# Kernel optimization log

Hardware: AMD Instinct MI355X
Metric: run time of the kernel (lower is better)

## Reference

```python
import jax, jax.numpy as jnp
import numpy as np

N, IN_DIM, EDGE_DIM = 100000, 64, 16
E = 1600000
H, C = 4, 16  # heads, out_dim per head; H*C = 64
K = 3
NEG_SLOPE = 0.2
LN_EPS = 1e-5


def setup_inputs() -> dict:
    key = jax.random.key(0)
    ks = jax.random.split(key, 16)
    s = 1.0 / np.sqrt(IN_DIM)
    se = 1.0 / np.sqrt(EDGE_DIM)
    HC = H * C
    return {
        "x": jax.random.normal(ks[0], (N, IN_DIM), jnp.float32),
        "edge_index": jax.random.randint(ks[1], (2, E), 0, N, jnp.int32),
        "edge_attr": jax.random.normal(ks[2], (E, EDGE_DIM), jnp.float32),
        "dist_to_boundary": jax.random.randint(ks[3], (N,), 0, K + 1, jnp.int32),
        # GATv2Conv params
        "W_l": jax.random.normal(ks[4], (IN_DIM, HC), jnp.float32) * s,
        "b_l": jnp.zeros((HC,), jnp.float32),
        "W_r": jax.random.normal(ks[5], (IN_DIM, HC), jnp.float32) * s,
        "b_r": jnp.zeros((HC,), jnp.float32),
        "W_e": jax.random.normal(ks[6], (EDGE_DIM, HC), jnp.float32) * se,
        "att": jax.random.normal(ks[7], (H, C), jnp.float32) * (1.0 / np.sqrt(C)),
        "bias": jnp.zeros((HC,), jnp.float32),
        # LayerNorm params
        "gamma": jnp.ones((HC,), jnp.float32),
        "beta": jnp.zeros((HC,), jnp.float32),
        # residual: in_dim == H*C -> Identity in original; identity-initialized Linear
        "W_res": jnp.eye(IN_DIM, HC, dtype=jnp.float32),
        "b_res": jnp.zeros((HC,), jnp.float32),
        "bias_per_hop": jnp.zeros((K + 1,), jnp.float32),
    }


def reference(x, edge_index, edge_attr, dist_to_boundary,
              W_l, b_l, W_r, b_r, W_e, att, bias,
              gamma, beta, W_res, b_res, bias_per_hop):
    n = x.shape[0]
    src, dst = edge_index[0], edge_index[1]

    # hop bias on edge features (module indexes edge_index[1])
    hop = jnp.clip(dist_to_boundary[dst], 0, K)
    ea = edge_attr + bias_per_hop[hop][:, None] * 0.1  # [E, edge_dim]

    # GATv2Conv (eval mode: no dropout)
    xl = (x @ W_l + b_l).reshape(n, H, C)
    xr = (x @ W_r + b_r).reshape(n, H, C)
    ee = (ea @ W_e).reshape(-1, H, C)
    m = xl[src] + xr[dst] + ee                      # [E,H,C]
    m = jnp.where(m > 0, m, NEG_SLOPE * m)          # leaky_relu
    logits = jnp.einsum('ehc,hc->eh', m, att)       # [E,H]

    # segment softmax over destination nodes
    amax = jax.ops.segment_max(logits, dst, num_segments=n)
    ex = jnp.exp(logits - amax[dst])
    den = jax.ops.segment_sum(ex, dst, num_segments=n)
    alpha = ex / (den[dst] + 1e-16)                 # [E,H]

    # weighted scatter-add of source features
    out = jax.ops.segment_sum(alpha[:, :, None] * xl[src], dst, num_segments=n)
    out = out.reshape(n, H * C) + bias

    # LayerNorm
    mu = out.mean(-1, keepdims=True)
    var = ((out - mu) ** 2).mean(-1, keepdims=True)
    out = (out - mu) / jnp.sqrt(var + LN_EPS) * gamma + beta

    # residual (Identity in original since in_dim == H*C; W_res is identity)
    return out + (x @ W_res + b_res)
```

## Files before the change

### kernel.cpp

```cpp
#include <hip/hip_runtime.h>
#include <math.h>

#define NEG_SLOPE 0.2f
#define LN_EPS 1e-5f
#define BUCKET 48

typedef __attribute__((ext_vector_type(2))) float f32x2;

template <int CTRL>
__device__ __forceinline__ float dpp_add(float x) {
    int s = __builtin_amdgcn_update_dpp(0, __float_as_int(x), CTRL, 0xF, 0xF, true);
    return x + __int_as_float(s);
}
__device__ __forceinline__ float row16_sum(float x) {
    x = dpp_add<0xB1>(x);
    x = dpp_add<0x4E>(x);
    x = dpp_add<0x124>(x);
    x = dpp_add<0x128>(x);
    return x;
}

__global__ __launch_bounds__(256) void prep(
    const float* __restrict__ x,
    const float* __restrict__ W_l, const float* __restrict__ b_l,
    const float* __restrict__ W_r, const float* __restrict__ b_r,
    const float* __restrict__ W_res, const float* __restrict__ b_res,
    const float* __restrict__ W_e,
    const int* __restrict__ dist, const float* __restrict__ bph,
    float* __restrict__ xl, float* __restrict__ xr, float* __restrict__ xres_out,
    const int* __restrict__ ei, int* __restrict__ counts, int2* __restrict__ bucket,
    int n, int E_) {
    __shared__ float sWl[4096];
    __shared__ float sWr[4096];
    __shared__ float sWs[4096];
    __shared__ float sx[256];
    for (int i = threadIdx.x; i < 4096; i += 256) {
        sWl[i] = W_l[i]; sWr[i] = W_r[i]; sWs[i] = W_res[i];
    }
    int lane = threadIdx.x & 63;
    int w = threadIdx.x >> 6;
    float bl = b_l[lane], br = b_r[lane], bs = b_res[lane];
    float wsum = 0.0f;
#pragma unroll
    for (int k = 0; k < 16; ++k) wsum += W_e[k * 64 + lane];
    __syncthreads();
    for (int base = blockIdx.x * 4; base < n; base += gridDim.x * 4) {
        __syncthreads();
        int r = base + w;
        if (r < n) sx[threadIdx.x] = x[(size_t)r * 64 + lane];
        __syncthreads();
        if (r < n) {
            float al = bl, ar = br, as_ = bs;
            const float* xv = &sx[w * 64];
#pragma unroll
            for (int k = 0; k < 64; ++k) {
                float xk = xv[k];
                al = fmaf(xk, sWl[k * 64 + lane], al);
                ar = fmaf(xk, sWr[k * 64 + lane], ar);
                as_ = fmaf(xk, sWs[k * 64 + lane], as_);
            }
            int hop = dist[r];
            hop = hop < 0 ? 0 : (hop > 3 ? 3 : hop);
            float hb = 0.1f * bph[hop];
            xl[(size_t)r * 64 + lane] = al;
            xr[(size_t)r * 64 + lane] = fmaf(hb, wsum, ar);
            xres_out[(size_t)r * 64 + lane] = as_;
        }
    }
    const int* di = ei + E_;
    for (int e = blockIdx.x * 256 + threadIdx.x; e < E_; e += gridDim.x * 256) {
        int dst = di[e];
        int src = ei[e];
        int pos = atomicAdd(&counts[dst], 1);
        pos = pos < BUCKET - 1 ? pos : BUCKET - 1;
        bucket[(size_t)dst * BUCKET + pos] = make_int2(e, src);
    }
}

#define LOAD_G(G, EA)                                                       \
    {                                                                       \
        int ec = __builtin_amdgcn_readfirstlane((EA).x);                    \
        const f32x2* p = (const f32x2*)(eattr + (size_t)ec * 16);           \
        _Pragma("unroll") for (int k = 0; k < 8; ++k) G[k] = p[k];          \
    }

#define PHASE(G, X, E, DEN, ACC, I)                                         \
    {                                                                       \
        f32x2 mm; mm.x = X + base; mm.y = 0.0f;                             \
        _Pragma("unroll") for (int k = 0; k < 8; ++k)                       \
            mm = __builtin_elementwise_fma(G[k], w2[k], mm);                \
        float m = mm.x + mm.y;                                              \
        m = fmaxf(m, NEG_SLOPE * m);                                        \
        float l = row16_sum(m * attv);      \
        l = (I) < cnt ? l : -1e30f;                                         \
        float ex = __builtin_amdgcn_exp2f(l);                               \
        DEN += ex;                                                          \
        ACC = fmaf(ex, X, ACC);                                             \
        X = xl[((unsigned)(E).y << 6) | lane];                              \
        LOAD_G(G, E);                                                       \
        int nx = (I) + 6; nx = nx > last ? last : nx;                       \
        E = bk[nx];                                                         \
    }

__global__ __launch_bounds__(256) void fused_gather(
    const int* __restrict__ counts, const int2* __restrict__ bucket,
    const float* __restrict__ eattr,
    const float* __restrict__ W_e, const float* __restrict__ att,
    const float* __restrict__ xl, const float* __restrict__ xr,
    const float* __restrict__ bias,
    const float* __restrict__ gamma, const float* __restrict__ beta,
    float* out, int n) {
    int lane = threadIdx.x & 63;
    float attv = att[lane] * 1.44269504f;
    float bi = bias[lane], g = gamma[lane], be = beta[lane];
    f32x2 w2[8];
#pragma unroll
    for (int k = 0; k < 8; ++k) {
        w2[k].x = W_e[(2 * k) * 64 + lane];
        w2[k].y = W_e[(2 * k + 1) * 64 + lane];
    }

    int wid = (blockIdx.x * blockDim.x + threadIdx.x) >> 6;
    int nw = (gridDim.x * blockDim.x) >> 6;
    for (int r = wid; r < n; r += nw) {
        int cnt = counts[r];
        float den0 = 0.0f, den1 = 0.0f, den2 = 0.0f;
        float acc0 = 0.0f, acc1 = 0.0f, acc2 = 0.0f;
        if (cnt > 0) {
            cnt = cnt < BUCKET ? cnt : BUCKET;
            float base = xr[((unsigned)r << 6) | lane];
            const int2* bk = bucket + (size_t)r * BUCKET;
            int last = cnt - 1;
            int i1 = 1 > last ? last : 1;
            int i2 = 2 > last ? last : 2;
            int i3 = 3 > last ? last : 3;
            int i4 = 4 > last ? last : 4;
            int i5 = 5 > last ? last : 5;
            int2 A0 = bk[0];
            int2 A1 = bk[i1];
            int2 A2 = bk[i2];
            int2 E0 = bk[i3];
            int2 E1 = bk[i4];
            int2 E2 = bk[i5];
            float X0 = xl[((unsigned)A0.y << 6) | lane];
            float X1 = xl[((unsigned)A1.y << 6) | lane];
            float X2 = xl[((unsigned)A2.y << 6) | lane];
            f32x2 G0[8], G1[8], G2[8];
            LOAD_G(G0, A0);
            LOAD_G(G1, A1);
            LOAD_G(G2, A2);
            for (int i = 0; i < cnt; i += 3) {
                PHASE(G0, X0, E0, den0, acc0, i)
                PHASE(G1, X1, E1, den1, acc1, i + 1)
                PHASE(G2, X2, E2, den2, acc2, i + 2)
            }
        }
        float den = (den0 + den1) + den2;
        float acc = (acc0 + acc1) + acc2;
        float v = acc / (den + 1e-16f) + bi;
        float s = row16_sum(v);
        s += __shfl_xor(s, 16, 64);
        s += __shfl_xor(s, 32, 64);
        float mu = s * (1.0f / 64.0f);
        float dd = v - mu;
        float q = row16_sum(dd * dd);
        q += __shfl_xor(q, 16, 64);
        q += __shfl_xor(q, 32, 64);
        float var = q * (1.0f / 64.0f);
        float nv = dd * rsqrtf(var + LN_EPS) * g + be;
        unsigned idx = ((unsigned)r << 6) | lane;
        out[idx] = nv + out[idx];
    }
}

extern "C" void kernel_launch(void* const* d_in, const int* in_sizes, int n_in,
                              void* d_out, int out_size, void* d_ws, size_t ws_size,
                              hipStream_t stream) {
    const float* x     = (const float*)d_in[0];
    const int*   ei    = (const int*)d_in[1];
    const float* eattr = (const float*)d_in[2];
    const int*   dist  = (const int*)d_in[3];
    const float* W_l   = (const float*)d_in[4];
    const float* b_l   = (const float*)d_in[5];
    const float* W_r   = (const float*)d_in[6];
    const float* b_r   = (const float*)d_in[7];
    const float* W_e   = (const float*)d_in[8];
    const float* att   = (const float*)d_in[9];
    const float* bias  = (const float*)d_in[10];
    const float* gamma = (const float*)d_in[11];
    const float* beta  = (const float*)d_in[12];
    const float* W_res = (const float*)d_in[13];
    const float* b_res = (const float*)d_in[14];
    const float* bph   = (const float*)d_in[15];

    int n  = in_sizes[0] / 64;
    int E_ = in_sizes[1] / 2;
    float* out = (float*)d_out;

    char* ws = (char*)d_ws;
    float* xl     = (float*)ws; ws += (size_t)n * 64 * 4;
    float* xr     = (float*)ws; ws += (size_t)n * 64 * 4;
    int2*  bucket = (int2*)ws;  ws += (size_t)n * BUCKET * 8;
    int*   counts = (int*)ws;   ws += (size_t)n * 4;

    hipMemsetAsync(counts, 0, (size_t)n * 4, stream);
    prep<<<2048, 256, 0, stream>>>(x, W_l, b_l, W_r, b_r, W_res, b_res, W_e,
                                   dist, bph, xl, xr, out, ei, counts, bucket, n, E_);
    fused_gather<<<4096, 256, 0, stream>>>(counts, bucket, eattr,
                                           W_e, att, xl, xr,
                                           bias, gamma, beta, out, n);
}
```

Before: 279.8 us.

## Deepen xl gather prefetch and compute two rows per wave in prep

In the fused gather, the xl row for each edge is now fetched one iteration earlier than the edge-attribute load, using an extra prefetch stage (XA/XB plus E/F index pipeline, lookahead 9). The aim is to hide gather latency better in this latency-bound loop. In prep, each wave now handles two node rows, so every weight value read from LDS is reused twice and LDS traffic per FMA drops. The cost is higher register pressure in both kernels, which may lower occupancy.

```diff
diff --git a/kernel.cpp b/kernel.cpp
--- a/kernel.cpp
+++ b/kernel.cpp
@@ -33,7 +33,7 @@
     __shared__ float sWl[4096];
     __shared__ float sWr[4096];
     __shared__ float sWs[4096];
-    __shared__ float sx[256];
+    __shared__ float sx[512];
     for (int i = threadIdx.x; i < 4096; i += 256) {
         sWl[i] = W_l[i]; sWr[i] = W_r[i]; sWs[i] = W_res[i];
     }
@@ -44,27 +44,49 @@
 #pragma unroll
     for (int k = 0; k < 16; ++k) wsum += W_e[k * 64 + lane];
     __syncthreads();
-    for (int base = blockIdx.x * 4; base < n; base += gridDim.x * 4) {
+    for (int base = blockIdx.x * 8; base < n; base += gridDim.x * 8) {
         __syncthreads();
-        int r = base + w;
-        if (r < n) sx[threadIdx.x] = x[(size_t)r * 64 + lane];
+        {
+            int idx = threadIdx.x;
+            int row = base + (idx >> 6);
+            if (row < n) sx[idx] = x[(size_t)row * 64 + (idx & 63)];
+            idx += 256;
+            row = base + (idx >> 6);
+            if (row < n) sx[idx] = x[(size_t)row * 64 + (idx & 63)];
+        }
         __syncthreads();
-        if (r < n) {
-            float al = bl, ar = br, as_ = bs;
-            const float* xv = &sx[w * 64];
+        int ra = base + w * 2;
+        int rb = ra + 1;
+        if (ra < n) {
+            float al0 = bl, ar0 = br, as0 = bs;
+            float al1 = bl, ar1 = br, as1 = bs;
+            const float* xa = &sx[(w * 2) * 64];
 #pragma unroll
             for (int k = 0; k < 64; ++k) {
-                float xk = xv[k];
-                al = fmaf(xk, sWl[k * 64 + lane], al);
-                ar = fmaf(xk, sWr[k * 64 + lane], ar);
-                as_ = fmaf(xk, sWs[k * 64 + lane], as_);
-            }
-            int hop = dist[r];
-            hop = hop < 0 ? 0 : (hop > 3 ? 3 : hop);
-            float hb = 0.1f * bph[hop];
-            xl[(size_t)r * 64 + lane] = al;
-            xr[(size_t)r * 64 + lane] = fmaf(hb, wsum, ar);
-            xres_out[(size_t)r * 64 + lane] = as_;
+                float wl = sWl[k * 64 + lane];
+                float wr_ = sWr[k * 64 + lane];
+                float ws_ = sWs[k * 64 + lane];
+                float x0 = xa[k];
+                float x1 = xa[k + 64];
+                al0 = fmaf(x0, wl, al0); ar0 = fmaf(x0, wr_, ar0); as0 = fmaf(x0, ws_, as0);
+                al1 = fmaf(x1, wl, al1); ar1 = fmaf(x1, wr_, ar1); as1 = fmaf(x1, ws_, as1);
+            }
+            {
+                int hop = dist[ra];
+                hop = hop < 0 ? 0 : (hop > 3 ? 3 : hop);
+                float hb = 0.1f * bph[hop];
+                xl[(size_t)ra * 64 + lane] = al0;
+                xr[(size_t)ra * 64 + lane] = fmaf(hb, wsum, ar0);
+                xres_out[(size_t)ra * 64 + lane] = as0;
+            }
+            if (rb < n) {
+                int hop = dist[rb];
+                hop = hop < 0 ? 0 : (hop > 3 ? 3 : hop);
+                float hb = 0.1f * bph[hop];
+                xl[(size_t)rb * 64 + lane] = al1;
+                xr[(size_t)rb * 64 + lane] = fmaf(hb, wsum, ar1);
+                xres_out[(size_t)rb * 64 + lane] = as1;
+            }
         }
     }
     const int* di = ei + E_;
@@ -84,9 +106,9 @@
         _Pragma("unroll") for (int k = 0; k < 8; ++k) G[k] = p[k];          \
     }
 
-#define PHASE(G, X, E, DEN, ACC, I)                                         \
+#define PHASE(G, XA, XB, E, F, DEN, ACC, I)                                 \
     {                                                                       \
-        f32x2 mm; mm.x = X + base; mm.y = 0.0f;                             \
+        f32x2 mm; mm.x = XA + base; mm.y = 0.0f;                            \
         _Pragma("unroll") for (int k = 0; k < 8; ++k)                       \
             mm = __builtin_elementwise_fma(G[k], w2[k], mm);                \
         float m = mm.x + mm.y;                                              \
@@ -95,11 +117,13 @@
         l = (I) < cnt ? l : -1e30f;                                         \
         float ex = __builtin_amdgcn_exp2f(l);                               \
         DEN += ex;                                                          \
-        ACC = fmaf(ex, X, ACC);                                             \
-        X = xl[((unsigned)(E).y << 6) | lane];                              \
+        ACC = fmaf(ex, XA, ACC);                                            \
+        XA = XB;                                                            \
+        XB = xl[((unsigned)(F).y << 6) | lane];                             \
         LOAD_G(G, E);                                                       \
-        int nx = (I) + 6; nx = nx > last ? last : nx;                       \
-        E = bk[nx];                                                         \
+        E = F;                                                              \
+        int nx = (I) + 9; nx = nx > last ? last : nx;                       \
+        F = bk[nx];                                                         \
     }
 
 __global__ __launch_bounds__(256) void fused_gather(
@@ -131,28 +155,37 @@
             float base = xr[((unsigned)r << 6) | lane];
             const int2* bk = bucket + (size_t)r * BUCKET;
             int last = cnt - 1;
-            int i1 = 1 > last ? last : 1;
-            int i2 = 2 > last ? last : 2;
-            int i3 = 3 > last ? last : 3;
-            int i4 = 4 > last ? last : 4;
-            int i5 = 5 > last ? last : 5;
-            int2 A0 = bk[0];
-            int2 A1 = bk[i1];
-            int2 A2 = bk[i2];
-            int2 E0 = bk[i3];
-            int2 E1 = bk[i4];
-            int2 E2 = bk[i5];
-            float X0 = xl[((unsigned)A0.y << 6) | lane];
-            float X1 = xl[((unsigned)A1.y << 6) | lane];
-            float X2 = xl[((unsigned)A2.y << 6) | lane];
+            int j1 = 1 > last ? last : 1;
+            int j2 = 2 > last ? last : 2;
+            int j3 = 3 > last ? last : 3;
+            int j4 = 4 > last ? last : 4;
+            int j5 = 5 > last ? last : 5;
+            int j6 = 6 > last ? last : 6;
+            int j7 = 7 > last ? last : 7;
+            int j8 = 8 > last ? last : 8;
+            int2 B0 = bk[0];
+            int2 B1 = bk[j1];
+            int2 B2 = bk[j2];
+            int2 E0 = bk[j3];
+            int2 E1 = bk[j4];
+            int2 E2 = bk[j5];
+            int2 F0 = bk[j6];
+            int2 F1 = bk[j7];
+            int2 F2 = bk[j8];
+            float Xa0 = xl[((unsigned)B0.y << 6) | lane];
+            float Xa1 = xl[((unsigned)B1.y << 6) | lane];
+            float Xa2 = xl[((unsigned)B2.y << 6) | lane];
+            float Xb0 = xl[((unsigned)E0.y << 6) | lane];
+            float Xb1 = xl[((unsigned)E1.y << 6) | lane];
+            float Xb2 = xl[((unsigned)E2.y << 6) | lane];
             f32x2 G0[8], G1[8], G2[8];
-            LOAD_G(G0, A0);
-            LOAD_G(G1, A1);
-            LOAD_G(G2, A2);
+            LOAD_G(G0, B0);
+            LOAD_G(G1, B1);
+            LOAD_G(G2, B2);
             for (int i = 0; i < cnt; i += 3) {
-                PHASE(G0, X0, E0, den0, acc0, i)
-                PHASE(G1, X1, E1, den1, acc1, i + 1)
-                PHASE(G2, X2, E2, den2, acc2, i + 2)
+                PHASE(G0, Xa0, Xb0, E0, F0, den0, acc0, i)
+                PHASE(G1, Xa1, Xb1, E1, F1, den1, acc1, i + 1)
+                PHASE(G2, Xa2, Xb2, E2, F2, den2, acc2, i + 2)
             }
         }
         float den = (den0 + den1) + den2;
```

New measurement: 324.3 us. +15.9%, slower.

## Split fused gather into edge-order logit kernel and destination gather kernel

Applied to the files above, without the earlier changes.

The fused per-destination kernel is split in two. A new edge_logits kernel walks edges in their original order, so the edge_attr reads are contiguous, and writes exp(logit) per edge and head to a workspace buffer. A second kernel gathers those values together with xl rows per destination, then does the normalization and LayerNorm. The aim is to avoid random 64-byte edge_attr reads in the gather, at the cost of an extra kernel launch, a 25.6MB intermediate write and read, and random xr[dst] gathers in the edge pass.

```diff
diff --git a/kernel.cpp b/kernel.cpp
--- a/kernel.cpp
+++ b/kernel.cpp
@@ -77,49 +77,102 @@
     }
 }
 
-#define LOAD_G(G, EA)                                                       \
+#define CL(J) ((J) > last ? last : (J))
+
+#define LLOAD_G(G, EE)                                                      \
     {                                                                       \
-        int ec = __builtin_amdgcn_readfirstlane((EA).x);                    \
-        const f32x2* p = (const f32x2*)(eattr + (size_t)ec * 16);           \
+        const f32x2* p = (const f32x2*)(eattr + (size_t)(EE) * 16);         \
         _Pragma("unroll") for (int k = 0; k < 8; ++k) G[k] = p[k];          \
     }
 
-#define PHASE(G, X, E, DEN, ACC, I)                                         \
+#define LPHASE(G, X, SS, DD, J)                                             \
     {                                                                       \
-        f32x2 mm; mm.x = X + base; mm.y = 0.0f;                             \
+        f32x2 mm; mm.x = X; mm.y = 0.0f;                                    \
         _Pragma("unroll") for (int k = 0; k < 8; ++k)                       \
             mm = __builtin_elementwise_fma(G[k], w2[k], mm);                \
         float m = mm.x + mm.y;                                              \
         m = fmaxf(m, NEG_SLOPE * m);                                        \
-        float l = row16_sum(m * attv);      \
-        l = (I) < cnt ? l : -1e30f;                                         \
+        float l = row16_sum(m * attv);                                      \
         float ex = __builtin_amdgcn_exp2f(l);                               \
-        DEN += ex;                                                          \
-        ACC = fmaf(ex, X, ACC);                                             \
-        X = xl[((unsigned)(E).y << 6) | lane];                              \
-        LOAD_G(G, E);                                                       \
-        int nx = (I) + 6; nx = nx > last ? last : nx;                       \
-        E = bk[nx];                                                         \
-    }
-
-__global__ __launch_bounds__(256) void fused_gather(
-    const int* __restrict__ counts, const int2* __restrict__ bucket,
-    const float* __restrict__ eattr,
+        if ((J) < len && (lane & 15) == 0)                                  \
+            exv[(size_t)(eb + (J)) * 4 + (lane >> 4)] = ex;                 \
+        int nj = CL((J) + 3);                                               \
+        LLOAD_G(G, eb + nj);                                                \
+        X = xl[((unsigned)SS << 6) | lane] + xr[((unsigned)DD << 6) | lane];\
+        int fj = eb + CL((J) + 6);                                          \
+        SS = ei[fj];                                                        \
+        DD = ei[E_ + fj];                                                   \
+    }
+
+__global__ __launch_bounds__(256) void edge_logits(
+    const int* __restrict__ ei, const float* __restrict__ eattr,
     const float* __restrict__ W_e, const float* __restrict__ att,
     const float* __restrict__ xl, const float* __restrict__ xr,
-    const float* __restrict__ bias,
-    const float* __restrict__ gamma, const float* __restrict__ beta,
-    float* out, int n) {
+    float* __restrict__ exv, int E_) {
     int lane = threadIdx.x & 63;
     float attv = att[lane] * 1.44269504f;
-    float bi = bias[lane], g = gamma[lane], be = beta[lane];
     f32x2 w2[8];
 #pragma unroll
     for (int k = 0; k < 8; ++k) {
         w2[k].x = W_e[(2 * k) * 64 + lane];
         w2[k].y = W_e[(2 * k + 1) * 64 + lane];
     }
-
+    int wid = (blockIdx.x * blockDim.x + threadIdx.x) >> 6;
+    int nw = (gridDim.x * blockDim.x) >> 6;
+    int chunk = (E_ + nw - 1) / nw;
+    int e0 = wid * chunk;
+    int e1 = e0 + chunk; if (e1 > E_) e1 = E_;
+    if (e0 >= e1) return;
+    int eb = __builtin_amdgcn_readfirstlane(e0);
+    int len = e1 - e0;
+    int last = len - 1;
+    int sA, dA, sB, dB, sC, dC;
+    float X0, X1, X2;
+    f32x2 G0[8], G1[8], G2[8];
+    {
+        int ja = 0, jb = CL(1), jc = CL(2);
+        int s0_ = ei[eb + ja], d0_ = ei[E_ + eb + ja];
+        int s1_ = ei[eb + jb], d1_ = ei[E_ + eb + jb];
+        int s2_ = ei[eb + jc], d2_ = ei[E_ + eb + jc];
+        X0 = xl[((unsigned)s0_ << 6) | lane] + xr[((unsigned)d0_ << 6) | lane];
+        X1 = xl[((unsigned)s1_ << 6) | lane] + xr[((unsigned)d1_ << 6) | lane];
+        X2 = xl[((unsigned)s2_ << 6) | lane] + xr[((unsigned)d2_ << 6) | lane];
+        LLOAD_G(G0, eb + ja);
+        LLOAD_G(G1, eb + jb);
+        LLOAD_G(G2, eb + jc);
+        int j3 = eb + CL(3), j4 = eb + CL(4), j5 = eb + CL(5);
+        sA = ei[j3]; dA = ei[E_ + j3];
+        sB = ei[j4]; dB = ei[E_ + j4];
+        sC = ei[j5]; dC = ei[E_ + j5];
+    }
+    for (int j = 0; j < len; j += 3) {
+        LPHASE(G0, X0, sA, dA, j)
+        LPHASE(G1, X1, sB, dB, j + 1)
+        LPHASE(G2, X2, sC, dC, j + 2)
+    }
+}
+
+#define GPHASE(EX, X, B, F, DEN, ACC, I)                                    \
+    {                                                                       \
+        float ex = (I) < cnt ? EX : 0.0f;                                   \
+        DEN += ex;                                                          \
+        ACC = fmaf(ex, X, ACC);                                             \
+        X = xl[((unsigned)(B).y << 6) | lane];                              \
+        EX = exv[(((unsigned)(B).x) << 2) + hsel];                          \
+        B = F;                                                              \
+        int nx = (I) + 9; nx = nx > lastj ? lastj : nx;                     \
+        F = bk[nx];                                                         \
+    }
+
+__global__ __launch_bounds__(256) void gather_ln(
+    const int* __restrict__ counts, const int2* __restrict__ bucket,
+    const float* __restrict__ exv, const float* __restrict__ xl,
+    const float* __restrict__ bias,
+    const float* __restrict__ gamma, const float* __restrict__ beta,
+    float* out, int n) {
+    int lane = threadIdx.x & 63;
+    unsigned hsel = lane >> 4;
+    float bi = bias[lane], g = gamma[lane], be = beta[lane];
     int wid = (blockIdx.x * blockDim.x + threadIdx.x) >> 6;
     int nw = (gridDim.x * blockDim.x) >> 6;
     for (int r = wid; r < n; r += nw) {
@@ -128,31 +181,35 @@
         float acc0 = 0.0f, acc1 = 0.0f, acc2 = 0.0f;
         if (cnt > 0) {
             cnt = cnt < BUCKET ? cnt : BUCKET;
-            float base = xr[((unsigned)r << 6) | lane];
             const int2* bk = bucket + (size_t)r * BUCKET;
-            int last = cnt - 1;
-            int i1 = 1 > last ? last : 1;
-            int i2 = 2 > last ? last : 2;
-            int i3 = 3 > last ? last : 3;
-            int i4 = 4 > last ? last : 4;
-            int i5 = 5 > last ? last : 5;
-            int2 A0 = bk[0];
-            int2 A1 = bk[i1];
-            int2 A2 = bk[i2];
-            int2 E0 = bk[i3];
-            int2 E1 = bk[i4];
-            int2 E2 = bk[i5];
-            float X0 = xl[((unsigned)A0.y << 6) | lane];
-            float X1 = xl[((unsigned)A1.y << 6) | lane];
-            float X2 = xl[((unsigned)A2.y << 6) | lane];
-            f32x2 G0[8], G1[8], G2[8];
-            LOAD_G(G0, A0);
-            LOAD_G(G1, A1);
-            LOAD_G(G2, A2);
+            int lastj = cnt - 1;
+            int j1 = 1 > lastj ? lastj : 1;
+            int j2 = 2 > lastj ? lastj : 2;
+            int j3 = 3 > lastj ? lastj : 3;
+            int j4 = 4 > lastj ? lastj : 4;
+            int j5 = 5 > lastj ? lastj : 5;
+            int j6 = 6 > lastj ? lastj : 6;
+            int j7 = 7 > lastj ? lastj : 7;
+            int j8 = 8 > lastj ? lastj : 8;
+            int2 b0 = bk[0];
+            int2 b1 = bk[j1];
+            int2 b2 = bk[j2];
+            int2 B0 = bk[j3];
+            int2 B1 = bk[j4];
+            int2 B2 = bk[j5];
+            int2 F0 = bk[j6];
+            int2 F1 = bk[j7];
+            int2 F2 = bk[j8];
+            float X0 = xl[((unsigned)b0.y << 6) | lane];
+            float X1 = xl[((unsigned)b1.y << 6) | lane];
+            float X2 = xl[((unsigned)b2.y << 6) | lane];
+            float EX0 = exv[(((unsigned)b0.x) << 2) + hsel];
+            float EX1 = exv[(((unsigned)b1.x) << 2) + hsel];
+            float EX2 = exv[(((unsigned)b2.x) << 2) + hsel];
             for (int i = 0; i < cnt; i += 3) {
-                PHASE(G0, X0, E0, den0, acc0, i)
-                PHASE(G1, X1, E1, den1, acc1, i + 1)
-                PHASE(G2, X2, E2, den2, acc2, i + 2)
+                GPHASE(EX0, X0, B0, F0, den0, acc0, i)
+                GPHASE(EX1, X1, B1, F1, den1, acc1, i + 1)
+                GPHASE(EX2, X2, B2, F2, den2, acc2, i + 2)
             }
         }
         float den = (den0 + den1) + den2;
@@ -201,12 +258,13 @@
     float* xl     = (float*)ws; ws += (size_t)n * 64 * 4;
     float* xr     = (float*)ws; ws += (size_t)n * 64 * 4;
     int2*  bucket = (int2*)ws;  ws += (size_t)n * BUCKET * 8;
+    float* exv    = (float*)ws; ws += (size_t)E_ * 4 * 4;
     int*   counts = (int*)ws;   ws += (size_t)n * 4;
 
     hipMemsetAsync(counts, 0, (size_t)n * 4, stream);
     prep<<<2048, 256, 0, stream>>>(x, W_l, b_l, W_r, b_r, W_res, b_res, W_e,
                                    dist, bph, xl, xr, out, ei, counts, bucket, n, E_);
-    fused_gather<<<4096, 256, 0, stream>>>(counts, bucket, eattr,
-                                           W_e, att, xl, xr,
-                                           bias, gamma, beta, out, n);
-}
+    edge_logits<<<4096, 256, 0, stream>>>(ei, eattr, W_e, att, xl, xr, exv, E_);
+    gather_ln<<<4096, 256, 0, stream>>>(counts, bucket, exv, xl,
+                                        bias, gamma, beta, out, n);
+}
```

Measured after the change: 516.3 us. 84.5% more time.

## Stage edge attributes into LDS via global_load_lds in double-buffered batches

Applied to the files above, without the earlier changes.

The gather kernel no longer loads each edge's 16 attribute floats with per-edge scalar loads. Each wave now issues one global_load_lds that copies four edges' attributes (64 floats) into a per-wave LDS slot, then reads them back as float4 vectors. The edge loop is rebuilt around batches of four edges with two LDS buffers and two accumulator chains, replacing the previous three-way software pipeline. This aims to use wide vector DMA instead of many scalar-cache loads for the large edge_attr stream. In exchange it adds LDS traffic and relies on correct wait ordering between the async LDS writes and the later reads.

```diff
diff --git a/kernel.cpp b/kernel.cpp
--- a/kernel.cpp
+++ b/kernel.cpp
@@ -6,6 +6,8 @@
 #define BUCKET 48
 
 typedef __attribute__((ext_vector_type(2))) float f32x2;
+typedef const float __attribute__((address_space(1))) gf32;
+typedef float __attribute__((address_space(3))) lf32;
 
 template <int CTRL>
 __device__ __forceinline__ float dpp_add(float x) {
@@ -77,29 +79,60 @@
     }
 }
 
-#define LOAD_G(G, EA)                                                       \
+
+#define RLOAD(R, BB)                                                        \
     {                                                                       \
-        int ec = __builtin_amdgcn_readfirstlane((EA).x);                    \
-        const f32x2* p = (const f32x2*)(eattr + (size_t)ec * 16);           \
-        _Pragma("unroll") for (int k = 0; k < 8; ++k) G[k] = p[k];          \
-    }
-
-#define PHASE(G, X, E, DEN, ACC, I)                                         \
+        int i0 = (BB) * 4;                                                  \
+        int k0 = i0 + 0 > last ? last : i0 + 0;                             \
+        int k1 = i0 + 1 > last ? last : i0 + 1;                             \
+        int k2 = i0 + 2 > last ? last : i0 + 2;                             \
+        int k3 = i0 + 3 > last ? last : i0 + 3;                             \
+        R[0] = bk[k0]; R[1] = bk[k1]; R[2] = bk[k2]; R[3] = bk[k3];         \
+    }
+
+#define ISSUE_GLDS(S, R)                                                    \
     {                                                                       \
-        f32x2 mm; mm.x = X + base; mm.y = 0.0f;                             \
-        _Pragma("unroll") for (int k = 0; k < 8; ++k)                       \
-            mm = __builtin_elementwise_fma(G[k], w2[k], mm);                \
-        float m = mm.x + mm.y;                                              \
-        m = fmaxf(m, NEG_SLOPE * m);                                        \
-        float l = row16_sum(m * attv);      \
-        l = (I) < cnt ? l : -1e30f;                                         \
-        float ex = __builtin_amdgcn_exp2f(l);                               \
-        DEN += ex;                                                          \
-        ACC = fmaf(ex, X, ACC);                                             \
-        X = xl[((unsigned)(E).y << 6) | lane];                              \
-        LOAD_G(G, E);                                                       \
-        int nx = (I) + 6; nx = nx > last ? last : nx;                       \
-        E = bk[nx];                                                         \
+        int e0 = R[0].x, e1 = R[1].x, e2 = R[2].x, e3 = R[3].x;             \
+        int eh = (lane & 16) ? e1 : e0;                                     \
+        int el = (lane & 16) ? e3 : e2;                                     \
+        int es = (lane & 32) ? el : eh;                                     \
+        const float* gp = eattr + (size_t)(unsigned)es * 16 + (lane & 15);  \
+        __builtin_amdgcn_global_load_lds((gf32*)gp, (lf32*)&S[w][0], 4, 0, 0); \
+    }
+
+#define XLOAD(X, R)                                                         \
+    X[0] = xl[((unsigned)R[0].y << 6) | lane];                              \
+    X[1] = xl[((unsigned)R[1].y << 6) | lane];                              \
+    X[2] = xl[((unsigned)R[2].y << 6) | lane];                              \
+    X[3] = xl[((unsigned)R[3].y << 6) | lane];
+
+#define PHASE(S, R, X, DEN, ACC, I)                                         \
+    {                                                                       \
+        _Pragma("unroll")                                                   \
+        for (int j = 0; j < 4; ++j) {                                       \
+            const float4* p = (const float4*)&S[w][j * 16];                 \
+            float4 qa = p[0], qb = p[1], qc = p[2], qd = p[3];              \
+            f32x2 mm; mm.x = X[j] + base; mm.y = 0.0f;                      \
+            f32x2 t;                                                        \
+            t.x = qa.x; t.y = qa.y; mm = __builtin_elementwise_fma(t, w2[0], mm); \
+            t.x = qa.z; t.y = qa.w; mm = __builtin_elementwise_fma(t, w2[1], mm); \
+            t.x = qb.x; t.y = qb.y; mm = __builtin_elementwise_fma(t, w2[2], mm); \
+            t.x = qb.z; t.y = qb.w; mm = __builtin_elementwise_fma(t, w2[3], mm); \
+            t.x = qc.x; t.y = qc.y; mm = __builtin_elementwise_fma(t, w2[4], mm); \
+            t.x = qc.z; t.y = qc.w; mm = __builtin_elementwise_fma(t, w2[5], mm); \
+            t.x = qd.x; t.y = qd.y; mm = __builtin_elementwise_fma(t, w2[6], mm); \
+            t.x = qd.z; t.y = qd.w; mm = __builtin_elementwise_fma(t, w2[7], mm); \
+            float m = mm.x + mm.y;                                          \
+            m = fmaxf(m, NEG_SLOPE * m);                                    \
+            float l = row16_sum(m * attv);                                  \
+            l = (4 * (I) + j) < cnt ? l : -1e30f;                           \
+            float ex = __builtin_amdgcn_exp2f(l);                           \
+            DEN += ex;                                                      \
+            ACC = fmaf(ex, X[j], ACC);                                      \
+        }                                                                   \
+        ISSUE_GLDS(S, R)        \
+        XLOAD(X, R)                              \
+        RLOAD(R, (I) + 4)                 \
     }
 
 __global__ __launch_bounds__(256) void fused_gather(
@@ -110,7 +143,10 @@
     const float* __restrict__ bias,
     const float* __restrict__ gamma, const float* __restrict__ beta,
     float* out, int n) {
+    __shared__ __align__(16) float sl0[4][64];
+    __shared__ __align__(16) float sl1[4][64];
     int lane = threadIdx.x & 63;
+    int w = threadIdx.x >> 6;
     float attv = att[lane] * 1.44269504f;
     float bi = bias[lane], g = gamma[lane], be = beta[lane];
     f32x2 w2[8];
@@ -124,39 +160,31 @@
     int nw = (gridDim.x * blockDim.x) >> 6;
     for (int r = wid; r < n; r += nw) {
         int cnt = counts[r];
-        float den0 = 0.0f, den1 = 0.0f, den2 = 0.0f;
-        float acc0 = 0.0f, acc1 = 0.0f, acc2 = 0.0f;
+        float den0 = 0.0f, den1 = 0.0f;
+        float acc0 = 0.0f, acc1 = 0.0f;
         if (cnt > 0) {
             cnt = cnt < BUCKET ? cnt : BUCKET;
             float base = xr[((unsigned)r << 6) | lane];
             const int2* bk = bucket + (size_t)r * BUCKET;
             int last = cnt - 1;
-            int i1 = 1 > last ? last : 1;
-            int i2 = 2 > last ? last : 2;
-            int i3 = 3 > last ? last : 3;
-            int i4 = 4 > last ? last : 4;
-            int i5 = 5 > last ? last : 5;
-            int2 A0 = bk[0];
-            int2 A1 = bk[i1];
-            int2 A2 = bk[i2];
-            int2 E0 = bk[i3];
-            int2 E1 = bk[i4];
-            int2 E2 = bk[i5];
-            float X0 = xl[((unsigned)A0.y << 6) | lane];
-            float X1 = xl[((unsigned)A1.y << 6) | lane];
-            float X2 = xl[((unsigned)A2.y << 6) | lane];
-            f32x2 G0[8], G1[8], G2[8];
-            LOAD_G(G0, A0);
-            LOAD_G(G1, A1);
-            LOAD_G(G2, A2);
-            for (int i = 0; i < cnt; i += 3) {
-                PHASE(G0, X0, E0, den0, acc0, i)
-                PHASE(G1, X1, E1, den1, acc1, i + 1)
-                PHASE(G2, X2, E2, den2, acc2, i + 2)
+            int B = (cnt + 3) >> 2;
+            int2 R0[4], R1[4];
+            float X0[4], X1[4];
+            RLOAD(R0, 0)
+            RLOAD(R1, 1)
+            ISSUE_GLDS(sl0, R0)
+            ISSUE_GLDS(sl1, R1)
+            XLOAD(X0, R0)
+            XLOAD(X1, R1)
+            RLOAD(R0, 2)
+            RLOAD(R1, 3)
+            for (int i = 0; i < B; i += 2) {
+                PHASE(sl0, R0, X0, den0, acc0, i)
+                PHASE(sl1, R1, X1, den1, acc1, i + 1)
             }
         }
-        float den = (den0 + den1) + den2;
-        float acc = (acc0 + acc1) + acc2;
+        float den = den0 + den1;
+        float acc = acc0 + acc1;
         float v = acc / (den + 1e-16f) + bi;
         float s = row16_sum(v);
         s += __shfl_xor(s, 16, 64);
```

Measured after the change: 318.7 us. 13.9% more time.
